# Kernel tuning notes

Measured on AMD Instinct MI355X. Metric: run time of the kernel, lower is better.

## Reference

```python
import jax, jax.numpy as jnp
import numpy as np

N, D_IN, D_BLOCK, D_OUT, E, K = 65536, 128, 256, 128, 8, 2


def setup_inputs() -> dict:
    key = jax.random.key(0)
    ks = jax.random.split(key, 8)
    s_in = 1.0 / np.sqrt(D_IN)
    s_h = 1.0 / np.sqrt(D_BLOCK)
    return {
        "x": jax.random.normal(ks[0], (N, D_IN), jnp.float32),
        "Wg": jax.random.normal(ks[1], (D_IN, E), jnp.float32) * s_in,
        "W1": jax.random.normal(ks[2], (E, D_IN, D_BLOCK), jnp.float32) * s_in,
        "b1": jax.random.normal(ks[3], (E, D_BLOCK), jnp.float32) * 0.01,
        "W2": jax.random.normal(ks[4], (E, D_BLOCK, D_BLOCK), jnp.float32) * s_h,
        "b2": jax.random.normal(ks[5], (E, D_BLOCK), jnp.float32) * 0.01,
        "Wo": jax.random.normal(ks[6], (D_BLOCK, D_OUT), jnp.float32) * s_h,
        "bo": jax.random.normal(ks[7], (D_OUT,), jnp.float32) * 0.01,
    }


def reference(x, Wg, W1, b1, W2, b2, Wo, bo):
    # Router: linear gate -> top-k -> softmax over the k selected logits,
    # scattered back to a dense [N, E] combine-weight matrix (zeros elsewhere).
    logits = x @ Wg                                   # [N, E]
    topv, topi = jax.lax.top_k(logits, K)             # [N, K]
    w_topk = jax.nn.softmax(topv, axis=-1)            # [N, K]
    onehot = jax.nn.one_hot(topi, E, dtype=x.dtype)   # [N, K, E]
    weights = jnp.einsum("nk,nke->ne", w_topk, onehot)  # [N, E]

    # Expert MLPs (n_blocks=2, ReLU, dropout=0 at eval), computed for all
    # experts over all tokens; unselected experts have weight 0, so the
    # weighted combine reproduces the original masked gather/scatter math.
    h = jax.nn.relu(jnp.einsum("nd,edh->enh", x, W1) + b1[:, None, :])   # [E,N,H]
    h = jax.nn.relu(jnp.einsum("enh,ehg->eng", h, W2) + b2[:, None, :])  # [E,N,H]
    y = jnp.einsum("enh,ho->eno", h, Wo) + bo                             # [E,N,O]

    # Weighted scatter-add combine: outs[n] = sum_e weights[n,e] * y[e,n]
    return jnp.einsum("ne,eno->no", weights, y)
```

## Files before the change

kernel.cpp:

```cpp
#include <hip/hip_runtime.h>
#include <math.h>

typedef unsigned short ushort_t;
typedef __attribute__((ext_vector_type(8))) short bf16x8;
typedef __attribute__((ext_vector_type(4))) short bf16x4;
typedef __attribute__((ext_vector_type(4))) float f32x4;
typedef __attribute__((ext_vector_type(8))) unsigned short u16x8;
typedef __attribute__((ext_vector_type(2))) unsigned int u32x2;
typedef __attribute__((ext_vector_type(4))) unsigned int u32x4;

#define N_TOK 65536
#define DIN 128
#define HD 256
#define DOUT 128
#define NEXP 8
#define MT 64
#define MAX_TILES (N_TOK / MT)

__device__ __forceinline__ unsigned short f2bf(float f) {
    union { float f; unsigned int i; } v; v.f = f;
    unsigned int i = v.i;
    return (unsigned short)((i + 0x7FFFu + ((i >> 16) & 1u)) >> 16);
}

#define RT_BLOCK 512
#define RT_TPB 64

__global__ __launch_bounds__(RT_BLOCK)
void router_kernel(const float* __restrict__ x,
                   const float* __restrict__ Wg,
                   const float* __restrict__ W1,
                   const float* __restrict__ W2,
                   const float* __restrict__ Wo,
                   const float* __restrict__ bo,
                   int* __restrict__ counts,
                   int* __restrict__ list_tok,
                   float* __restrict__ list_w,
                   ushort_t* __restrict__ wt1f,
                   ushort_t* __restrict__ wt2f,
                   ushort_t* __restrict__ wotf,
                   float* __restrict__ out) {
    __shared__ float wgsT[NEXP * 132];
    __shared__ int lcnt[NEXP];
    __shared__ int lbase[NEXP];
    int tid = threadIdx.x;
    if (tid < NEXP) lcnt[tid] = 0;
    for (int i = tid; i < DIN * NEXP; i += RT_BLOCK) {
        int ee = i & 7, k = i >> 3;
        wgsT[ee * 132 + k] = Wg[i];
    }
    {
        const float4* bo4 = (const float4*)bo;
        float4* ob = (float4*)(out + (size_t)blockIdx.x * RT_TPB * DOUT);
#pragma unroll
        for (int i = 0; i < 4; i++) {
            int idx = i * RT_BLOCK + tid;
            ob[idx] = bo4[idx & 31];
        }
    }
    if (blockIdx.x < 200) {
        int id = blockIdx.x * RT_BLOCK + tid;
        const float* src; ushort_t* dst; int Nn, ksteps, c;
        if (id < 32768) {
            int ee = id >> 12; c = id & 4095;
            Nn = HD; ksteps = 4; src = W1 + (size_t)ee * DIN * HD; dst = wt1f + (size_t)id * 8;
        } else if (id < 98304) {
            int t = id - 32768; int ee = t >> 13; c = t & 8191;
            Nn = HD; ksteps = 8; src = W2 + (size_t)ee * HD * HD; dst = wt2f + (size_t)t * 8;
        } else {
            int t = id - 98304; c = t;
            Nn = DOUT; ksteps = 8; src = Wo; dst = wotf + (size_t)t * 8;
        }
        int L = c & 63; int kc = c >> 6;
        int kstep = kc % ksteps; int ntile = kc / ksteps;
        int qq = L >> 4, mm = L & 15;
        int n = ntile * 16 + mm; int k0 = kstep * 32 + qq * 8;
        u16x8 v;
#pragma unroll
        for (int j = 0; j < 8; j++) v[j] = f2bf(src[(size_t)(k0 + j) * Nn + n]);
        *(u16x8*)dst = v;
    }
    __syncthreads();

    int e = tid & 7;
    int tl = tid >> 3;
    int n = blockIdx.x * RT_TPB + tl;
    const float4* xr = (const float4*)(x + (size_t)n * DIN);
    const float4* wv4 = (const float4*)(wgsT + e * 132);
    float lg = 0.f;
#pragma unroll
    for (int kk = 0; kk < 32; kk++) {
        float4 xv = xr[kk];
        float4 wv = wv4[kk];
        lg += xv.x * wv.x;
        lg += xv.y * wv.y;
        lg += xv.z * wv.z;
        lg += xv.w * wv.w;
    }
    float v0 = lg; int e0 = e;
#pragma unroll
    for (int d = 1; d < 8; d <<= 1) {
        float ov = __shfl_xor(v0, d, 64);
        int oe = __shfl_xor(e0, d, 64);
        if (ov > v0 || (ov == v0 && oe < e0)) { v0 = ov; e0 = oe; }
    }
    float mv = (e == e0) ? -3.0e38f : lg;
    float v1 = mv; int e1 = e;
#pragma unroll
    for (int d = 1; d < 8; d <<= 1) {
        float ov = __shfl_xor(v1, d, 64);
        int oe = __shfl_xor(e1, d, 64);
        if (ov > v1 || (ov == v1 && oe < e1)) { v1 = ov; e1 = oe; }
    }
    float t = expf(v1 - v0);
    float inv = 1.0f / (1.0f + t);
    float w0 = inv, w1 = t * inv;

    bool writer = (e == 0);
    int p0 = 0, p1 = 0;
    if (writer) {
        p0 = atomicAdd(&lcnt[e0], 1);
        p1 = atomicAdd(&lcnt[e1], 1);
    }
    __syncthreads();
    if (tid < NEXP) lbase[tid] = atomicAdd(&counts[tid], lcnt[tid]);
    __syncthreads();
    if (writer) {
        int q0 = lbase[e0] + p0;
        list_tok[e0 * N_TOK + q0] = n;
        list_w[e0 * N_TOK + q0] = w0;
        int q1 = lbase[e1] + p1;
        list_tok[e1 * N_TOK + q1] = n;
        list_w[e1 * N_TOK + q1] = w1;
    }
}

__global__ __launch_bounds__(256, 3)
void expert_kernel(const float* __restrict__ x,
                   const int* __restrict__ counts,
                   const int* __restrict__ list_tok,
                   const float* __restrict__ list_w,
                   const ushort_t* __restrict__ wt1f,
                   const ushort_t* __restrict__ wt2f,
                   const ushort_t* __restrict__ wotf,
                   const float* __restrict__ b1,
                   const float* __restrict__ b2,
                   float* __restrict__ out) {
    int e = blockIdx.x & 7;
    int tile = blockIdx.x >> 3;
    int cnt = counts[e];
    int base = tile * MT;
    if (base >= cnt) return;
    int rows = cnt - base; if (rows > MT) rows = MT;

    __shared__ __align__(16) ushort_t bufA[8192];
    __shared__ __align__(16) ushort_t bufH[16384];
    __shared__ int toks_s[MT];
    __shared__ float wts_s[MT];

    int tid = threadIdx.x;
    int lane = tid & 63;
    int w = tid >> 6;
    int q = lane >> 4;
    int mcol = lane & 15;

    if (tid < MT) {
        int rr = tid < rows ? tid : rows - 1;
        toks_s[tid] = list_tok[(size_t)e * N_TOK + base + rr];
        wts_s[tid] = list_w[(size_t)e * N_TOK + base + rr];
    }

    float bias1[4], bias2[4];
#pragma unroll
    for (int nt = 0; nt < 4; nt++) {
        int nn = (w * 4 + nt) * 16 + mcol;
        bias1[nt] = b1[e * HD + nn];
        bias2[nt] = b2[e * HD + nn];
    }
    const bf16x8* B1 = (const bf16x8*)(wt1f + (size_t)e * 4096 * 8);
    bf16x8 b1r[2][4];
#pragma unroll
    for (int nt = 0; nt < 4; nt++) b1r[0][nt] = B1[((w * 4 + nt) * 4 + 0) * 64 + lane];

    for (int c = tid; c < 1024; c += 256) {
        int row = c >> 4;
        int kchunk = c & 15;
        int rr = row < rows ? row : rows - 1;
        int tok = list_tok[(size_t)e * N_TOK + base + rr];
        const float4* src = (const float4*)(x + (size_t)tok * DIN + kchunk * 8);
        float4 lo = src[0], hi = src[1];
        unsigned p0, p1, p2, p3;
        asm("v_cvt_pk_bf16_f32 %0, %1, %2" : "=v"(p0) : "v"(lo.x), "v"(lo.y));
        asm("v_cvt_pk_bf16_f32 %0, %1, %2" : "=v"(p1) : "v"(lo.z), "v"(lo.w));
        asm("v_cvt_pk_bf16_f32 %0, %1, %2" : "=v"(p2) : "v"(hi.x), "v"(hi.y));
        asm("v_cvt_pk_bf16_f32 %0, %1, %2" : "=v"(p3) : "v"(hi.z), "v"(hi.w));
        int kstep = kchunk >> 2, qq = kchunk & 3;
        int dchunk = (kstep * 4 + (row >> 4)) * 64 + qq * 16 + (row & 15);
        u32x4 v; v.x = p0; v.y = p1; v.z = p2; v.w = p3;
        *(u32x4*)(&bufA[dchunk * 8]) = v;
    }
    __syncthreads();

    const bf16x8* Albs = (const bf16x8*)bufA;

    f32x4 acc[4][4];
#pragma unroll
    for (int mt = 0; mt < 4; mt++)
#pragma unroll
        for (int nt = 0; nt < 4; nt++) acc[mt][nt] = (f32x4){0.f, 0.f, 0.f, 0.f};
#pragma unroll
    for (int kstep = 0; kstep < 4; kstep++) {
        const int cur = kstep & 1, nxt = cur ^ 1;
        if (kstep < 3) {
#pragma unroll
            for (int nt = 0; nt < 4; nt++)
                b1r[nxt][nt] = B1[((w * 4 + nt) * 4 + kstep + 1) * 64 + lane];
        }
        bf16x8 a[4];
#pragma unroll
        for (int mt = 0; mt < 4; mt++) a[mt] = Albs[(kstep * 4 + mt) * 64 + lane];
#pragma unroll
        for (int nt = 0; nt < 4; nt++)
#pragma unroll
            for (int mt = 0; mt < 4; mt++)
                acc[mt][nt] = __builtin_amdgcn_mfma_f32_16x16x32_bf16(a[mt], b1r[cur][nt], acc[mt][nt], 0, 0, 0);
    }

    const bf16x8* B2 = (const bf16x8*)(wt2f + (size_t)e * 8192 * 8);
    bf16x8 b2r[2][4];
#pragma unroll
    for (int nt = 0; nt < 4; nt++) b2r[0][nt] = B2[((w * 4 + nt) * 8 + 0) * 64 + lane];

#pragma unroll
    for (int nt = 0; nt < 4; nt++) {
        int off0 = w * 2048 + nt * 512 + (mcol >> 2) * 128 + (mcol & 3) * 32 + q * 8;
#pragma unroll
        for (int mt = 0; mt < 4; mt++) {
            float v0 = acc[mt][nt][0] + bias1[nt]; v0 = v0 > 0.f ? v0 : 0.f;
            float v1 = acc[mt][nt][1] + bias1[nt]; v1 = v1 > 0.f ? v1 : 0.f;
            float v2 = acc[mt][nt][2] + bias1[nt]; v2 = v2 > 0.f ? v2 : 0.f;
            float v3 = acc[mt][nt][3] + bias1[nt]; v3 = v3 > 0.f ? v3 : 0.f;
            unsigned d0, d1;
            asm("v_cvt_pk_bf16_f32 %0, %1, %2" : "=v"(d0) : "v"(v0), "v"(v1));
            asm("v_cvt_pk_bf16_f32 %0, %1, %2" : "=v"(d1) : "v"(v2), "v"(v3));
            u32x2 dd; dd.x = d0; dd.y = d1;
            *(u32x2*)(&bufH[(mt * 8192 + off0) >> 1]) = dd;
        }
    }
    __syncthreads();

    unsigned trb = ((unsigned)(size_t)(void*)bufH) + (unsigned)(q * 256 + mcol * 8);

    f32x4 acc2[4][4];
#pragma unroll
    for (int mt = 0; mt < 4; mt++)
#pragma unroll
        for (int nt = 0; nt < 4; nt++) acc2[mt][nt] = (f32x4){0.f, 0.f, 0.f, 0.f};
#pragma unroll
    for (int kstep = 0; kstep < 8; kstep++) {
        const int cur = kstep & 1, nxt = cur ^ 1;
        if (kstep < 7) {
#pragma unroll
            for (int nt = 0; nt < 4; nt++)
                b2r[nxt][nt] = B2[((w * 4 + nt) * 8 + kstep + 1) * 64 + lane];
        }
        bf16x8 a[4];
#pragma unroll
        for (int mt = 0; mt < 4; mt++) {
            bf16x4 lo, hi;
            unsigned ad = trb + (unsigned)(mt * 8192 + kstep * 1024);
            asm volatile("ds_read_b64_tr_b16 %0, %2\n\t"
                         "ds_read_b64_tr_b16 %1, %2 offset:128"
                         : "=&v"(lo), "=&v"(hi) : "v"(ad));
            a[mt] = __builtin_shufflevector(lo, hi, 0, 1, 2, 3, 4, 5, 6, 7);
        }
        asm volatile("s_waitcnt lgkmcnt(0)" ::: "memory");
        __builtin_amdgcn_sched_barrier(0);
#pragma unroll
        for (int nt = 0; nt < 4; nt++)
#pragma unroll
            for (int mt = 0; mt < 4; mt++)
                acc2[mt][nt] = __builtin_amdgcn_mfma_f32_16x16x32_bf16(a[mt], b2r[cur][nt], acc2[mt][nt], 0, 0, 0);
    }
    __syncthreads();

    const bf16x8* B3 = (const bf16x8*)wotf;
    bf16x8 b3r[2][2];
#pragma unroll
    for (int nt = 0; nt < 2; nt++) b3r[0][nt] = B3[((w * 2 + nt) * 8 + 0) * 64 + lane];

#pragma unroll
    for (int nt = 0; nt < 4; nt++) {
        int off0 = w * 2048 + nt * 512 + (mcol >> 2) * 128 + (mcol & 3) * 32 + q * 8;
#pragma unroll
        for (int mt = 0; mt < 4; mt++) {
            float v0 = acc2[mt][nt][0] + bias2[nt]; v0 = v0 > 0.f ? v0 : 0.f;
            float v1 = acc2[mt][nt][1] + bias2[nt]; v1 = v1 > 0.f ? v1 : 0.f;
            float v2 = acc2[mt][nt][2] + bias2[nt]; v2 = v2 > 0.f ? v2 : 0.f;
            float v3 = acc2[mt][nt][3] + bias2[nt]; v3 = v3 > 0.f ? v3 : 0.f;
            unsigned d0, d1;
            asm("v_cvt_pk_bf16_f32 %0, %1, %2" : "=v"(d0) : "v"(v0), "v"(v1));
            asm("v_cvt_pk_bf16_f32 %0, %1, %2" : "=v"(d1) : "v"(v2), "v"(v3));
            u32x2 dd; dd.x = d0; dd.y = d1;
            *(u32x2*)(&bufH[(mt * 8192 + off0) >> 1]) = dd;
        }
    }
    __syncthreads();

    f32x4 acc3[4][2];
#pragma unroll
    for (int mt = 0; mt < 4; mt++)
#pragma unroll
        for (int nt = 0; nt < 2; nt++) acc3[mt][nt] = (f32x4){0.f, 0.f, 0.f, 0.f};
#pragma unroll
    for (int kstep = 0; kstep < 8; kstep++) {
        const int cur = kstep & 1, nxt = cur ^ 1;
        if (kstep < 7) {
#pragma unroll
            for (int nt = 0; nt < 2; nt++)
                b3r[nxt][nt] = B3[((w * 2 + nt) * 8 + kstep + 1) * 64 + lane];
        }
        bf16x8 a[4];
#pragma unroll
        for (int mt = 0; mt < 4; mt++) {
            bf16x4 lo, hi;
            unsigned ad = trb + (unsigned)(mt * 8192 + kstep * 1024);
            asm volatile("ds_read_b64_tr_b16 %0, %2\n\t"
                         "ds_read_b64_tr_b16 %1, %2 offset:128"
                         : "=&v"(lo), "=&v"(hi) : "v"(ad));
            a[mt] = __builtin_shufflevector(lo, hi, 0, 1, 2, 3, 4, 5, 6, 7);
        }
        asm volatile("s_waitcnt lgkmcnt(0)" ::: "memory");
        __builtin_amdgcn_sched_barrier(0);
#pragma unroll
        for (int nt = 0; nt < 2; nt++)
#pragma unroll
            for (int mt = 0; mt < 4; mt++)
                acc3[mt][nt] = __builtin_amdgcn_mfma_f32_16x16x32_bf16(a[mt], b3r[cur][nt], acc3[mt][nt], 0, 0, 0);
    }
#pragma unroll
    for (int mt = 0; mt < 4; mt++) {
#pragma unroll
        for (int r = 0; r < 4; r++) {
            int row = mt * 16 + q * 4 + r;
            if (row < rows) {
                int tok = toks_s[row];
                float wgt = wts_s[row];
                float* dst = out + (size_t)tok * DOUT;
#pragma unroll
                for (int nt = 0; nt < 2; nt++) {
                    int col = (w * 2 + nt) * 16 + mcol;
                    atomicAdd(&dst[col], wgt * acc3[mt][nt][r]);
                }
            }
        }
    }
}

extern "C" void kernel_launch(void* const* d_in, const int* in_sizes, int n_in,
                              void* d_out, int out_size, void* d_ws, size_t ws_size,
                              hipStream_t stream) {
    const float* x  = (const float*)d_in[0];
    const float* Wg = (const float*)d_in[1];
    const float* W1 = (const float*)d_in[2];
    const float* b1 = (const float*)d_in[3];
    const float* W2 = (const float*)d_in[4];
    const float* b2 = (const float*)d_in[5];
    const float* Wo = (const float*)d_in[6];
    const float* bo = (const float*)d_in[7];
    float* out = (float*)d_out;

    char* ws = (char*)d_ws;
    size_t off = 0;
    int* counts    = (int*)(ws + off);    off += 256;
    int* list_tok  = (int*)(ws + off);    off += (size_t)NEXP * N_TOK * 4;
    float* list_w  = (float*)(ws + off);  off += (size_t)NEXP * N_TOK * 4;
    ushort_t* wt1f = (ushort_t*)(ws + off); off += (size_t)NEXP * DIN * HD * 2;
    ushort_t* wt2f = (ushort_t*)(ws + off); off += (size_t)NEXP * HD * HD * 2;
    ushort_t* wotf = (ushort_t*)(ws + off); off += (size_t)HD * DOUT * 2;

    hipMemsetAsync(counts, 0, 256, stream);
    router_kernel<<<N_TOK / RT_TPB, RT_BLOCK, 0, stream>>>(
        x, Wg, W1, W2, Wo, bo, counts, list_tok, list_w, wt1f, wt2f, wotf, out);
    expert_kernel<<<NEXP * MAX_TILES, 256, 0, stream>>>(x, counts, list_tok, list_w,
                                                        wt1f, wt2f, wotf, b1, b2, out);
}
```

Baseline: 178.8 us.

## Persistent expert tiles with swapped GEMM operands, single LDS buffer, padded counters

The expert kernel now runs a fixed grid of 320 blocks per expert that loop over token tiles, instead of one block per possible tile with most exiting early. The GEMMs swap operand roles: weights become the A operand, and activations are read from one shared LDS buffer written in transposed layout. This drops the second LDS buffer and the ds_read_tr loads, and raises the occupancy hint from 3 to 4. The router doubles its block size and pads the per-expert atomic counters to separate cache lines. The risks are extra barriers per tile and register pressure at the higher occupancy target.

```diff
diff --git a/kernel.cpp b/kernel.cpp
--- a/kernel.cpp
+++ b/kernel.cpp
@@ -3,7 +3,6 @@
 
 typedef unsigned short ushort_t;
 typedef __attribute__((ext_vector_type(8))) short bf16x8;
-typedef __attribute__((ext_vector_type(4))) short bf16x4;
 typedef __attribute__((ext_vector_type(4))) float f32x4;
 typedef __attribute__((ext_vector_type(8))) unsigned short u16x8;
 typedef __attribute__((ext_vector_type(2))) unsigned int u32x2;
@@ -15,7 +14,7 @@
 #define DOUT 128
 #define NEXP 8
 #define MT 64
-#define MAX_TILES (N_TOK / MT)
+#define NB_T 320
 
 __device__ __forceinline__ unsigned short f2bf(float f) {
     union { float f; unsigned int i; } v; v.f = f;
@@ -23,8 +22,8 @@
     return (unsigned short)((i + 0x7FFFu + ((i >> 16) & 1u)) >> 16);
 }
 
-#define RT_BLOCK 512
-#define RT_TPB 64
+#define RT_BLOCK 1024
+#define RT_TPB 128
 
 __global__ __launch_bounds__(RT_BLOCK)
 void router_kernel(const float* __restrict__ x,
@@ -45,9 +44,9 @@
     __shared__ int lbase[NEXP];
     int tid = threadIdx.x;
     if (tid < NEXP) lcnt[tid] = 0;
-    for (int i = tid; i < DIN * NEXP; i += RT_BLOCK) {
-        int ee = i & 7, k = i >> 3;
-        wgsT[ee * 132 + k] = Wg[i];
+    if (tid < DIN * NEXP) {
+        int ee = tid & 7, k = tid >> 3;
+        wgsT[ee * 132 + k] = Wg[tid];
     }
     {
         const float4* bo4 = (const float4*)bo;
@@ -58,7 +57,7 @@
             ob[idx] = bo4[idx & 31];
         }
     }
-    if (blockIdx.x < 200) {
+    if (blockIdx.x < 100) {
         int id = blockIdx.x * RT_BLOCK + tid;
         const float* src; ushort_t* dst; int Nn, ksteps, c;
         if (id < 32768) {
@@ -123,7 +122,7 @@
         p1 = atomicAdd(&lcnt[e1], 1);
     }
     __syncthreads();
-    if (tid < NEXP) lbase[tid] = atomicAdd(&counts[tid], lcnt[tid]);
+    if (tid < NEXP) lbase[tid] = atomicAdd(&counts[tid * 32], lcnt[tid]);
     __syncthreads();
     if (writer) {
         int q0 = lbase[e0] + p0;
@@ -135,7 +134,7 @@
     }
 }
 
-__global__ __launch_bounds__(256, 3)
+__global__ __launch_bounds__(256, 4)
 void expert_kernel(const float* __restrict__ x,
                    const int* __restrict__ counts,
                    const int* __restrict__ list_tok,
@@ -147,13 +146,9 @@
                    const float* __restrict__ b2,
                    float* __restrict__ out) {
     int e = blockIdx.x & 7;
-    int tile = blockIdx.x >> 3;
-    int cnt = counts[e];
-    int base = tile * MT;
-    if (base >= cnt) return;
-    int rows = cnt - base; if (rows > MT) rows = MT;
-
-    __shared__ __align__(16) ushort_t bufA[8192];
+    int t0 = blockIdx.x >> 3;
+    int cnt = counts[e * 32];
+
     __shared__ __align__(16) ushort_t bufH[16384];
     __shared__ int toks_s[MT];
     __shared__ float wts_s[MT];
@@ -164,193 +159,187 @@
     int q = lane >> 4;
     int mcol = lane & 15;
 
-    if (tid < MT) {
-        int rr = tid < rows ? tid : rows - 1;
-        toks_s[tid] = list_tok[(size_t)e * N_TOK + base + rr];
-        wts_s[tid] = list_w[(size_t)e * N_TOK + base + rr];
-    }
-
-    float bias1[4], bias2[4];
-#pragma unroll
-    for (int nt = 0; nt < 4; nt++) {
-        int nn = (w * 4 + nt) * 16 + mcol;
-        bias1[nt] = b1[e * HD + nn];
-        bias2[nt] = b2[e * HD + nn];
-    }
-    const bf16x8* B1 = (const bf16x8*)(wt1f + (size_t)e * 4096 * 8);
-    bf16x8 b1r[2][4];
-#pragma unroll
-    for (int nt = 0; nt < 4; nt++) b1r[0][nt] = B1[((w * 4 + nt) * 4 + 0) * 64 + lane];
-
-    for (int c = tid; c < 1024; c += 256) {
-        int row = c >> 4;
-        int kchunk = c & 15;
-        int rr = row < rows ? row : rows - 1;
-        int tok = list_tok[(size_t)e * N_TOK + base + rr];
-        const float4* src = (const float4*)(x + (size_t)tok * DIN + kchunk * 8);
-        float4 lo = src[0], hi = src[1];
-        unsigned p0, p1, p2, p3;
-        asm("v_cvt_pk_bf16_f32 %0, %1, %2" : "=v"(p0) : "v"(lo.x), "v"(lo.y));
-        asm("v_cvt_pk_bf16_f32 %0, %1, %2" : "=v"(p1) : "v"(lo.z), "v"(lo.w));
-        asm("v_cvt_pk_bf16_f32 %0, %1, %2" : "=v"(p2) : "v"(hi.x), "v"(hi.y));
-        asm("v_cvt_pk_bf16_f32 %0, %1, %2" : "=v"(p3) : "v"(hi.z), "v"(hi.w));
-        int kstep = kchunk >> 2, qq = kchunk & 3;
-        int dchunk = (kstep * 4 + (row >> 4)) * 64 + qq * 16 + (row & 15);
-        u32x4 v; v.x = p0; v.y = p1; v.z = p2; v.w = p3;
-        *(u32x4*)(&bufA[dchunk * 8]) = v;
-    }
-    __syncthreads();
-
-    const bf16x8* Albs = (const bf16x8*)bufA;
-
-    f32x4 acc[4][4];
-#pragma unroll
-    for (int mt = 0; mt < 4; mt++)
-#pragma unroll
-        for (int nt = 0; nt < 4; nt++) acc[mt][nt] = (f32x4){0.f, 0.f, 0.f, 0.f};
-#pragma unroll
-    for (int kstep = 0; kstep < 4; kstep++) {
-        const int cur = kstep & 1, nxt = cur ^ 1;
-        if (kstep < 3) {
-#pragma unroll
-            for (int nt = 0; nt < 4; nt++)
-                b1r[nxt][nt] = B1[((w * 4 + nt) * 4 + kstep + 1) * 64 + lane];
-        }
-        bf16x8 a[4];
-#pragma unroll
-        for (int mt = 0; mt < 4; mt++) a[mt] = Albs[(kstep * 4 + mt) * 64 + lane];
-#pragma unroll
-        for (int nt = 0; nt < 4; nt++)
-#pragma unroll
-            for (int mt = 0; mt < 4; mt++)
-                acc[mt][nt] = __builtin_amdgcn_mfma_f32_16x16x32_bf16(a[mt], b1r[cur][nt], acc[mt][nt], 0, 0, 0);
-    }
-
-    const bf16x8* B2 = (const bf16x8*)(wt2f + (size_t)e * 8192 * 8);
-    bf16x8 b2r[2][4];
-#pragma unroll
-    for (int nt = 0; nt < 4; nt++) b2r[0][nt] = B2[((w * 4 + nt) * 8 + 0) * 64 + lane];
-
-#pragma unroll
-    for (int nt = 0; nt < 4; nt++) {
-        int off0 = w * 2048 + nt * 512 + (mcol >> 2) * 128 + (mcol & 3) * 32 + q * 8;
+    const bf16x8* W1A = (const bf16x8*)(wt1f + (size_t)e * 4096 * 8);
+    const bf16x8* W2A = (const bf16x8*)(wt2f + (size_t)e * 8192 * 8);
+    const bf16x8* WoB = (const bf16x8*)wotf;
+    const bf16x8* Hlbs = (const bf16x8*)bufH;
+
+    float4 b1v[4], b2v[4];
+#pragma unroll
+    for (int rtl = 0; rtl < 4; rtl++) {
+        b1v[rtl] = *(const float4*)(b1 + e * HD + w * 64 + rtl * 16 + q * 4);
+        b2v[rtl] = *(const float4*)(b2 + e * HD + w * 64 + rtl * 16 + q * 4);
+    }
+
+    for (int tile = t0; tile * MT < cnt; tile += NB_T) {
+        int base = tile * MT;
+        int rows = cnt - base; if (rows > MT) rows = MT;
+
+        __syncthreads();
+
+        if (tid < MT) {
+            int rr = tid < rows ? tid : rows - 1;
+            toks_s[tid] = list_tok[(size_t)e * N_TOK + base + rr];
+            wts_s[tid] = list_w[(size_t)e * N_TOK + base + rr];
+        }
+
+        bf16x8 a1r[2][4];
+#pragma unroll
+        for (int rtl = 0; rtl < 4; rtl++)
+            a1r[0][rtl] = W1A[((w * 4 + rtl) * 4 + 0) * 64 + lane];
+
+        for (int c = tid; c < 1024; c += 256) {
+            int row = c >> 4;
+            int kchunk = c & 15;
+            int rr = row < rows ? row : rows - 1;
+            int tok = list_tok[(size_t)e * N_TOK + base + rr];
+            const float4* src = (const float4*)(x + (size_t)tok * DIN + kchunk * 8);
+            float4 lo = src[0], hi = src[1];
+            unsigned p0, p1, p2, p3;
+            asm("v_cvt_pk_bf16_f32 %0, %1, %2" : "=v"(p0) : "v"(lo.x), "v"(lo.y));
+            asm("v_cvt_pk_bf16_f32 %0, %1, %2" : "=v"(p1) : "v"(lo.z), "v"(lo.w));
+            asm("v_cvt_pk_bf16_f32 %0, %1, %2" : "=v"(p2) : "v"(hi.x), "v"(hi.y));
+            asm("v_cvt_pk_bf16_f32 %0, %1, %2" : "=v"(p3) : "v"(hi.z), "v"(hi.w));
+            int dchunk = ((kchunk >> 2) * 4 + (row >> 4)) * 64 + (kchunk & 3) * 16 + (row & 15);
+            u32x4 v; v.x = p0; v.y = p1; v.z = p2; v.w = p3;
+            *(u32x4*)(&bufH[dchunk * 8]) = v;
+        }
+        __syncthreads();
+
+        f32x4 acc[4][4];
+#pragma unroll
+        for (int rtl = 0; rtl < 4; rtl++)
+#pragma unroll
+            for (int ct = 0; ct < 4; ct++) acc[rtl][ct] = (f32x4){0.f, 0.f, 0.f, 0.f};
+#pragma unroll
+        for (int ks = 0; ks < 4; ks++) {
+            const int cur = ks & 1, nxt = cur ^ 1;
+            if (ks < 3) {
+#pragma unroll
+                for (int rtl = 0; rtl < 4; rtl++)
+                    a1r[nxt][rtl] = W1A[((w * 4 + rtl) * 4 + ks + 1) * 64 + lane];
+            }
+            bf16x8 bf_[4];
+#pragma unroll
+            for (int ct = 0; ct < 4; ct++) bf_[ct] = Hlbs[(ks * 4 + ct) * 64 + lane];
+#pragma unroll
+            for (int rtl = 0; rtl < 4; rtl++)
+#pragma unroll
+                for (int ct = 0; ct < 4; ct++)
+                    acc[rtl][ct] = __builtin_amdgcn_mfma_f32_16x16x32_bf16(a1r[cur][rtl], bf_[ct], acc[rtl][ct], 0, 0, 0);
+        }
+        bf16x8 a2r[2][4];
+#pragma unroll
+        for (int rtl = 0; rtl < 4; rtl++)
+            a2r[0][rtl] = W2A[((w * 4 + rtl) * 8 + 0) * 64 + lane];
+
+        __syncthreads();
+
+#pragma unroll
+        for (int rtl = 0; rtl < 4; rtl++) {
+            int ks2 = w * 2 + (rtl >> 1);
+            int q2 = (rtl * 2 + (q >> 1)) & 3;
+            int uoff = (ks2 * 4 * 64 + q2 * 16 + mcol) * 8 + (q & 1) * 4;
+#pragma unroll
+            for (int ct = 0; ct < 4; ct++) {
+                float v0 = acc[rtl][ct][0] + b1v[rtl].x; v0 = v0 > 0.f ? v0 : 0.f;
+                float v1 = acc[rtl][ct][1] + b1v[rtl].y; v1 = v1 > 0.f ? v1 : 0.f;
+                float v2 = acc[rtl][ct][2] + b1v[rtl].z; v2 = v2 > 0.f ? v2 : 0.f;
+                float v3 = acc[rtl][ct][3] + b1v[rtl].w; v3 = v3 > 0.f ? v3 : 0.f;
+                unsigned d0, d1;
+                asm("v_cvt_pk_bf16_f32 %0, %1, %2" : "=v"(d0) : "v"(v0), "v"(v1));
+                asm("v_cvt_pk_bf16_f32 %0, %1, %2" : "=v"(d1) : "v"(v2), "v"(v3));
+                u32x2 dd; dd.x = d0; dd.y = d1;
+                *(u32x2*)(&bufH[uoff + ct * 512]) = dd;
+            }
+        }
+        __syncthreads();
+
+        f32x4 acc2[4][4];
+#pragma unroll
+        for (int rtl = 0; rtl < 4; rtl++)
+#pragma unroll
+            for (int ct = 0; ct < 4; ct++) acc2[rtl][ct] = (f32x4){0.f, 0.f, 0.f, 0.f};
+#pragma unroll
+        for (int ks = 0; ks < 8; ks++) {
+            const int cur = ks & 1, nxt = cur ^ 1;
+            if (ks < 7) {
+#pragma unroll
+                for (int rtl = 0; rtl < 4; rtl++)
+                    a2r[nxt][rtl] = W2A[((w * 4 + rtl) * 8 + ks + 1) * 64 + lane];
+            }
+            bf16x8 bf_[4];
+#pragma unroll
+            for (int ct = 0; ct < 4; ct++) bf_[ct] = Hlbs[(ks * 4 + ct) * 64 + lane];
+#pragma unroll
+            for (int rtl = 0; rtl < 4; rtl++)
+#pragma unroll
+                for (int ct = 0; ct < 4; ct++)
+                    acc2[rtl][ct] = __builtin_amdgcn_mfma_f32_16x16x32_bf16(a2r[cur][rtl], bf_[ct], acc2[rtl][ct], 0, 0, 0);
+        }
+        bf16x8 b3r[2][2];
+#pragma unroll
+        for (int nt = 0; nt < 2; nt++)
+            b3r[0][nt] = WoB[((w * 2 + nt) * 8 + 0) * 64 + lane];
+
+        __syncthreads();
+
+#pragma unroll
+        for (int rtl = 0; rtl < 4; rtl++) {
+            int ks2 = w * 2 + (rtl >> 1);
+            int q2 = (rtl * 2 + (q >> 1)) & 3;
+            int uoff = (ks2 * 4 * 64 + q2 * 16 + mcol) * 8 + (q & 1) * 4;
+#pragma unroll
+            for (int ct = 0; ct < 4; ct++) {
+                float v0 = acc2[rtl][ct][0] + b2v[rtl].x; v0 = v0 > 0.f ? v0 : 0.f;
+                float v1 = acc2[rtl][ct][1] + b2v[rtl].y; v1 = v1 > 0.f ? v1 : 0.f;
+                float v2 = acc2[rtl][ct][2] + b2v[rtl].z; v2 = v2 > 0.f ? v2 : 0.f;
+                float v3 = acc2[rtl][ct][3] + b2v[rtl].w; v3 = v3 > 0.f ? v3 : 0.f;
+                unsigned d0, d1;
+                asm("v_cvt_pk_bf16_f32 %0, %1, %2" : "=v"(d0) : "v"(v0), "v"(v1));
+                asm("v_cvt_pk_bf16_f32 %0, %1, %2" : "=v"(d1) : "v"(v2), "v"(v3));
+                u32x2 dd; dd.x = d0; dd.y = d1;
+                *(u32x2*)(&bufH[uoff + ct * 512]) = dd;
+            }
+        }
+        __syncthreads();
+
+        f32x4 acc3[4][2];
+#pragma unroll
+        for (int mt = 0; mt < 4; mt++)
+#pragma unroll
+            for (int nt = 0; nt < 2; nt++) acc3[mt][nt] = (f32x4){0.f, 0.f, 0.f, 0.f};
+#pragma unroll
+        for (int ks = 0; ks < 8; ks++) {
+            const int cur = ks & 1, nxt = cur ^ 1;
+            if (ks < 7) {
+#pragma unroll
+                for (int nt = 0; nt < 2; nt++)
+                    b3r[nxt][nt] = WoB[((w * 2 + nt) * 8 + ks + 1) * 64 + lane];
+            }
+            bf16x8 af_[4];
+#pragma unroll
+            for (int mt = 0; mt < 4; mt++) af_[mt] = Hlbs[(ks * 4 + mt) * 64 + lane];
+#pragma unroll
+            for (int nt = 0; nt < 2; nt++)
+#pragma unroll
+                for (int mt = 0; mt < 4; mt++)
+                    acc3[mt][nt] = __builtin_amdgcn_mfma_f32_16x16x32_bf16(af_[mt], b3r[cur][nt], acc3[mt][nt], 0, 0, 0);
+        }
 #pragma unroll
         for (int mt = 0; mt < 4; mt++) {
-            float v0 = acc[mt][nt][0] + bias1[nt]; v0 = v0 > 0.f ? v0 : 0.f;
-            float v1 = acc[mt][nt][1] + bias1[nt]; v1 = v1 > 0.f ? v1 : 0.f;
-            float v2 = acc[mt][nt][2] + bias1[nt]; v2 = v2 > 0.f ? v2 : 0.f;
-            float v3 = acc[mt][nt][3] + bias1[nt]; v3 = v3 > 0.f ? v3 : 0.f;
-            unsigned d0, d1;
-            asm("v_cvt_pk_bf16_f32 %0, %1, %2" : "=v"(d0) : "v"(v0), "v"(v1));
-            asm("v_cvt_pk_bf16_f32 %0, %1, %2" : "=v"(d1) : "v"(v2), "v"(v3));
-            u32x2 dd; dd.x = d0; dd.y = d1;
-            *(u32x2*)(&bufH[(mt * 8192 + off0) >> 1]) = dd;
-        }
-    }
-    __syncthreads();
-
-    unsigned trb = ((unsigned)(size_t)(void*)bufH) + (unsigned)(q * 256 + mcol * 8);
-
-    f32x4 acc2[4][4];
-#pragma unroll
-    for (int mt = 0; mt < 4; mt++)
-#pragma unroll
-        for (int nt = 0; nt < 4; nt++) acc2[mt][nt] = (f32x4){0.f, 0.f, 0.f, 0.f};
-#pragma unroll
-    for (int kstep = 0; kstep < 8; kstep++) {
-        const int cur = kstep & 1, nxt = cur ^ 1;
-        if (kstep < 7) {
-#pragma unroll
-            for (int nt = 0; nt < 4; nt++)
-                b2r[nxt][nt] = B2[((w * 4 + nt) * 8 + kstep + 1) * 64 + lane];
-        }
-        bf16x8 a[4];
-#pragma unroll
-        for (int mt = 0; mt < 4; mt++) {
-            bf16x4 lo, hi;
-            unsigned ad = trb + (unsigned)(mt * 8192 + kstep * 1024);
-            asm volatile("ds_read_b64_tr_b16 %0, %2\n\t"
-                         "ds_read_b64_tr_b16 %1, %2 offset:128"
-                         : "=&v"(lo), "=&v"(hi) : "v"(ad));
-            a[mt] = __builtin_shufflevector(lo, hi, 0, 1, 2, 3, 4, 5, 6, 7);
-        }
-        asm volatile("s_waitcnt lgkmcnt(0)" ::: "memory");
-        __builtin_amdgcn_sched_barrier(0);
-#pragma unroll
-        for (int nt = 0; nt < 4; nt++)
-#pragma unroll
-            for (int mt = 0; mt < 4; mt++)
-                acc2[mt][nt] = __builtin_amdgcn_mfma_f32_16x16x32_bf16(a[mt], b2r[cur][nt], acc2[mt][nt], 0, 0, 0);
-    }
-    __syncthreads();
-
-    const bf16x8* B3 = (const bf16x8*)wotf;
-    bf16x8 b3r[2][2];
-#pragma unroll
-    for (int nt = 0; nt < 2; nt++) b3r[0][nt] = B3[((w * 2 + nt) * 8 + 0) * 64 + lane];
-
-#pragma unroll
-    for (int nt = 0; nt < 4; nt++) {
-        int off0 = w * 2048 + nt * 512 + (mcol >> 2) * 128 + (mcol & 3) * 32 + q * 8;
-#pragma unroll
-        for (int mt = 0; mt < 4; mt++) {
-            float v0 = acc2[mt][nt][0] + bias2[nt]; v0 = v0 > 0.f ? v0 : 0.f;
-            float v1 = acc2[mt][nt][1] + bias2[nt]; v1 = v1 > 0.f ? v1 : 0.f;
-            float v2 = acc2[mt][nt][2] + bias2[nt]; v2 = v2 > 0.f ? v2 : 0.f;
-            float v3 = acc2[mt][nt][3] + bias2[nt]; v3 = v3 > 0.f ? v3 : 0.f;
-            unsigned d0, d1;
-            asm("v_cvt_pk_bf16_f32 %0, %1, %2" : "=v"(d0) : "v"(v0), "v"(v1));
-            asm("v_cvt_pk_bf16_f32 %0, %1, %2" : "=v"(d1) : "v"(v2), "v"(v3));
-            u32x2 dd; dd.x = d0; dd.y = d1;
-            *(u32x2*)(&bufH[(mt * 8192 + off0) >> 1]) = dd;
-        }
-    }
-    __syncthreads();
-
-    f32x4 acc3[4][2];
-#pragma unroll
-    for (int mt = 0; mt < 4; mt++)
-#pragma unroll
-        for (int nt = 0; nt < 2; nt++) acc3[mt][nt] = (f32x4){0.f, 0.f, 0.f, 0.f};
-#pragma unroll
-    for (int kstep = 0; kstep < 8; kstep++) {
-        const int cur = kstep & 1, nxt = cur ^ 1;
-        if (kstep < 7) {
-#pragma unroll
-            for (int nt = 0; nt < 2; nt++)
-                b3r[nxt][nt] = B3[((w * 2 + nt) * 8 + kstep + 1) * 64 + lane];
-        }
-        bf16x8 a[4];
-#pragma unroll
-        for (int mt = 0; mt < 4; mt++) {
-            bf16x4 lo, hi;
-            unsigned ad = trb + (unsigned)(mt * 8192 + kstep * 1024);
-            asm volatile("ds_read_b64_tr_b16 %0, %2\n\t"
-                         "ds_read_b64_tr_b16 %1, %2 offset:128"
-                         : "=&v"(lo), "=&v"(hi) : "v"(ad));
-            a[mt] = __builtin_shufflevector(lo, hi, 0, 1, 2, 3, 4, 5, 6, 7);
-        }
-        asm volatile("s_waitcnt lgkmcnt(0)" ::: "memory");
-        __builtin_amdgcn_sched_barrier(0);
-#pragma unroll
-        for (int nt = 0; nt < 2; nt++)
-#pragma unroll
-            for (int mt = 0; mt < 4; mt++)
-                acc3[mt][nt] = __builtin_amdgcn_mfma_f32_16x16x32_bf16(a[mt], b3r[cur][nt], acc3[mt][nt], 0, 0, 0);
-    }
-#pragma unroll
-    for (int mt = 0; mt < 4; mt++) {
-#pragma unroll
-        for (int r = 0; r < 4; r++) {
-            int row = mt * 16 + q * 4 + r;
-            if (row < rows) {
-                int tok = toks_s[row];
-                float wgt = wts_s[row];
-                float* dst = out + (size_t)tok * DOUT;
-#pragma unroll
-                for (int nt = 0; nt < 2; nt++) {
-                    int col = (w * 2 + nt) * 16 + mcol;
-                    atomicAdd(&dst[col], wgt * acc3[mt][nt][r]);
+#pragma unroll
+            for (int r = 0; r < 4; r++) {
+                int row = mt * 16 + q * 4 + r;
+                if (row < rows) {
+                    int tok = toks_s[row];
+                    float wgt = wts_s[row];
+                    float* dst = out + (size_t)tok * DOUT;
+#pragma unroll
+                    for (int nt = 0; nt < 2; nt++) {
+                        int col = (w * 2 + nt) * 16 + mcol;
+                        atomicAdd(&dst[col], wgt * acc3[mt][nt][r]);
+                    }
                 }
             }
         }
@@ -372,16 +361,16 @@
 
     char* ws = (char*)d_ws;
     size_t off = 0;
-    int* counts    = (int*)(ws + off);    off += 256;
+    int* counts    = (int*)(ws + off);    off += 1024;
     int* list_tok  = (int*)(ws + off);    off += (size_t)NEXP * N_TOK * 4;
     float* list_w  = (float*)(ws + off);  off += (size_t)NEXP * N_TOK * 4;
     ushort_t* wt1f = (ushort_t*)(ws + off); off += (size_t)NEXP * DIN * HD * 2;
     ushort_t* wt2f = (ushort_t*)(ws + off); off += (size_t)NEXP * HD * HD * 2;
     ushort_t* wotf = (ushort_t*)(ws + off); off += (size_t)HD * DOUT * 2;
 
-    hipMemsetAsync(counts, 0, 256, stream);
+    hipMemsetAsync(counts, 0, 1024, stream);
     router_kernel<<<N_TOK / RT_TPB, RT_BLOCK, 0, stream>>>(
         x, Wg, W1, W2, Wo, bo, counts, list_tok, list_w, wt1f, wt2f, wotf, out);
-    expert_kernel<<<NEXP * MAX_TILES, 256, 0, stream>>>(x, counts, list_tok, list_w,
-                                                        wt1f, wt2f, wotf, b1, b2, out);
+    expert_kernel<<<NEXP * NB_T, 256, 0, stream>>>(x, counts, list_tok, list_w,
+                                                   wt1f, wt2f, wotf, b1, b2, out);
 }
```

Measured after the change: 321.1 us. 1.8x slower.
